# Kernel tuning notes

Measured on AMD Instinct MI355X. Metric: run time of the kernel, lower is better.

## Reference

```python
import jax, jax.numpy as jnp
import numpy as np

EPS = 1e-3  # tfa GroupNormalization default epsilon
H = 8       # num heads


def group_norm(x, gamma, beta):
    # x: [..., E]; per-sample group norm over each group of head_dim channels
    lead, E = x.shape[:-1], x.shape[-1]
    D = E // H
    xg = x.reshape(lead + (H, D))
    mu = xg.mean(-1, keepdims=True)
    var = xg.var(-1, keepdims=True)
    xg = (xg - mu) * jax.lax.rsqrt(var + EPS)
    xg = xg * gamma.reshape(H, D) + beta.reshape(H, D)
    return xg.reshape(lead + (E,))


def in_proj(x, W, b, gamma, beta):
    # Dense -> CELU(alpha=1) == ELU -> GroupNorm(groups=H)
    return group_norm(jax.nn.elu(x @ W + b), gamma, beta)


def setup_inputs() -> dict:
    B, M, E, MID = 16, 2048, 1024, 64
    D = E // H
    ks = jax.random.split(jax.random.key(0), 16)
    w = lambda k, shape: jax.random.normal(k, shape, jnp.float32) * 0.02
    inp = {
        "query": jax.random.normal(ks[0], (B, E), jnp.float32),
        "key": jax.random.normal(ks[1], (B * M, E), jnp.float32),
        "mask": jnp.ones((B, M), jnp.float32),
        "value1": jax.random.normal(ks[2], (B, E), jnp.float32),
        "value2": jax.random.normal(ks[3], (B * M, E), jnp.float32),
        # four in-projection layers: Dense(E,E) + GroupNorm gamma/beta
        "Wq": w(ks[4], (E, E)), "bq": jnp.zeros((E,), jnp.float32), "gq": jnp.ones((E,), jnp.float32), "Bq": jnp.zeros((E,), jnp.float32),
        "Wk": w(ks[5], (E, E)), "bk": jnp.zeros((E,), jnp.float32), "gk": jnp.ones((E,), jnp.float32), "Bk": jnp.zeros((E,), jnp.float32),
        "Wv1": w(ks[6], (E, E)), "bv1": jnp.zeros((E,), jnp.float32), "gv1": jnp.ones((E,), jnp.float32), "Bv1": jnp.zeros((E,), jnp.float32),
        "Wv2": w(ks[7], (E, E)), "bv2": jnp.zeros((E,), jnp.float32), "gv2": jnp.ones((E,), jnp.float32), "Bv2": jnp.zeros((E,), jnp.float32),
        # XLASCAtt: basic Dense(head_dim->64)+ReLU; last Dense(64->1); last2 Dense(64->head_dim)
        "Wb": w(ks[8], (D, MID)), "bb": jnp.zeros((MID,), jnp.float32),
        "Wl1": w(ks[9], (MID, 1)), "bl1": jnp.zeros((1,), jnp.float32),
        "Wl2": w(ks[10], (MID, D)), "bl2": jnp.zeros((D,), jnp.float32),
    }
    return inp


def reference(query, key, mask, value1, value2,
              Wq, bq, gq, Bq, Wk, bk, gk, Bk,
              Wv1, bv1, gv1, Bv1, Wv2, bv2, gv2, Bv2,
              Wb, bb, Wl1, bl1, Wl2, bl2):
    B, E = query.shape
    D = E // H
    # in-projections
    q = in_proj(query, Wq, bq, gq, Bq).reshape(B, H, D)            # [B,H,D]
    v1 = in_proj(value1, Wv1, bv1, gv1, Bv1).reshape(B, H, D)      # [B,H,D]
    k = in_proj(key, Wk, bk, gk, Bk).reshape(B, -1, H, D).transpose(0, 2, 1, 3)       # [B,H,M,D]
    v2 = in_proj(value2, Wv2, bv2, gv2, Bv2).reshape(B, -1, H, D).transpose(0, 2, 1, 3)  # [B,H,M,D]

    # low-rank bilinear attention map: elementwise q*k per head
    att_map = q[:, :, None, :] * k                                 # [B,H,M,D]
    basic = jax.nn.relu(att_map @ Wb + bb)                         # [B,H,M,MID]

    # masked mean-pool over memory positions
    m_ext = mask[:, None, :, None]                                 # [B,1,M,1]
    pool = (basic * m_ext).sum(-2) / m_ext.sum(-2)                 # [B,H,MID]

    # spatial attention (softmax over M) and channel gate (sigmoid)
    alpha_sp = (basic @ Wl1 + bl1)[..., 0]                         # [B,H,M]
    alpha_sp = jnp.where(mask[:, None, :] == 0, -1e9, alpha_sp)
    alpha_sp = jax.nn.softmax(alpha_sp, axis=-1)
    alpha_ch = jax.nn.sigmoid(pool @ Wl2 + bl2)                    # [B,H,D]

    v2_agg = jnp.einsum('bhm,bhmd->bhd', alpha_sp, v2)             # [B,H,D]
    attn = v1 * v2_agg * alpha_ch                                  # [B,H,D]
    return attn.reshape(B, H * D)
```

## Files before the change

kernel.cpp:

```cpp
#include <hip/hip_runtime.h>
#include <hip/hip_bf16.h>
#include <math.h>

typedef __attribute__((ext_vector_type(8))) short bf16x8;
typedef __attribute__((ext_vector_type(4))) float f32x4;
typedef __attribute__((ext_vector_type(8))) unsigned short u16x8;

typedef const float* fptr;
typedef const unsigned short* bfp;

__device__ inline float b2f(unsigned short u) {
    union { unsigned int i; float f; } v; v.i = ((unsigned int)u) << 16; return v.f;
}
__device__ inline unsigned short f2b(float x) {
    __hip_bfloat16 h = __float2bfloat16(x);
    return *(unsigned short*)&h;
}
__device__ inline float elu_f(float x) { return x > 0.f ? x : __expf(x) - 1.f; }

__device__ inline void load_lds16(const void* g, void* l) {
    __builtin_amdgcn_global_load_lds(
        (const __attribute__((address_space(1))) unsigned int*)g,
        (__attribute__((address_space(3))) unsigned int*)l, 16, 0, 0);
}

__global__ __launch_bounds__(256) void prep(
    fptr key, fptr value2, unsigned short* AbfK, unsigned short* AbfV2,
    fptr Wk, fptr Wv2, unsigned short* WtK, unsigned short* WtV2,
    fptr Wb, unsigned short* Wbt,
    fptr query, fptr Wq, fptr bq, fptr gq, fptr Bq,
    fptr value1, fptr Wv1, fptr bv1, fptr gv1, fptr Bv1,
    float* qws, float* v1ws)
{
    __shared__ __align__(16) char smem[16640];
    int blk = blockIdx.x, t = threadIdx.x;

    if (blk == 0) {
        unsigned short* tb = (unsigned short*)smem;
        for (int i = 0; i < 32; i++) {
            int idx = i * 256 + t;
            tb[(idx & 63) * 128 + (idx >> 6)] = f2b(Wb[idx]);
        }
        __syncthreads();
        for (int i = 0; i < 4; i++) {
            int o = (i * 256 + t) * 8;
            *(u16x8*)&Wbt[o] = *(const u16x8*)&tb[o];
        }
        return;
    }
    if (blk < 257) {
        float* xs = (float*)smem;
        float (*part)[128] = (float (*)[128])(smem + 4096);
        float (*r4)[2] = (float (*)[2])(smem + 4096 + 1024);
        int idx = blk - 1;
        int hgrp = idx & 7;
        int row  = (idx >> 3) & 15;
        int which = idx >> 7;
        fptr x  = which ? value1 : query;
        fptr W  = which ? Wv1 : Wq;
        fptr bi = which ? bv1 : bq;
        fptr g  = which ? gv1 : gq;
        fptr be = which ? Bv1 : Bq;
        float* outp = which ? v1ws : qws;
        int lane = t & 63, wv = t >> 6;
        for (int i = t; i < 1024; i += 256) xs[i] = x[row * 1024 + i];
        __syncthreads();
        int cl = t & 127, kh = t >> 7;
        int col = hgrp * 128 + cl;
        float acc = 0.f;
        const float* wp = W + (size_t)(kh * 512) * 1024 + col;
        for (int k = 0; k < 512; k++) acc += xs[kh * 512 + k] * wp[(size_t)k * 1024];
        part[kh][cl] = acc;
        __syncthreads();
        float e = 0.f;
        if (t < 128) e = elu_f(part[0][t] + part[1][t] + bi[col]);
        float s = e, ss = e * e;
        for (int m = 32; m > 0; m >>= 1) { s += __shfl_xor(s, m); ss += __shfl_xor(ss, m); }
        if (lane == 0) { r4[wv][0] = s; r4[wv][1] = ss; }
        __syncthreads();
        float S  = r4[0][0] + r4[1][0] + r4[2][0] + r4[3][0];
        float SS = r4[0][1] + r4[1][1] + r4[2][1] + r4[3][1];
        float mean = S * (1.f / 128.f);
        float var  = SS * (1.f / 128.f) - mean * mean;
        float inv  = rsqrtf(var + 1e-3f);
        if (t < 128) outp[row * 1024 + col] = (e - mean) * inv * g[col] + be[col];
        return;
    }
    if (blk < 769) {
        float (*tl)[65] = (float (*)[65])smem;
        int idx = blk - 257;
        fptr W = (idx >> 8) ? Wv2 : Wk;
        unsigned short* Wt = (idx >> 8) ? WtV2 : WtK;
        int k0 = ((idx >> 4) & 15) * 64, n0 = (idx & 15) * 64;
        #pragma unroll
        for (int i = 0; i < 16; i++) {
            int kl = i * 4 + (t >> 6), nl = t & 63;
            tl[kl][nl] = W[(size_t)(k0 + kl) * 1024 + n0 + nl];
        }
        __syncthreads();
        #pragma unroll
        for (int i = 0; i < 2; i++) {
            int nl = i * 32 + (t >> 3), kl8 = (t & 7) * 8;
            u16x8 o;
            #pragma unroll
            for (int e = 0; e < 8; e++) o[e] = f2b(tl[kl8 + e][nl]);
            *(u16x8*)&Wt[(size_t)(n0 + nl) * 1024 + k0 + kl8] = o;
        }
        return;
    }
    {
        int idx = blk - 769;
        fptr A = (idx < 2048) ? key : value2;
        unsigned short* Bp = (idx < 2048) ? AbfK : AbfV2;
        size_t base = (size_t)(idx & 2047) * 16384 + (size_t)t * 8;
        #pragma unroll
        for (int i = 0; i < 8; i++) {
            size_t e = base + (size_t)i * 2048;
            const float4* ap = (const float4*)(A + e);
            float4 a0 = ap[0], a1 = ap[1];
            u16x8 p = { f2b(a0.x), f2b(a0.y), f2b(a0.z), f2b(a0.w),
                        f2b(a1.x), f2b(a1.y), f2b(a1.z), f2b(a1.w) };
            *(u16x8*)(Bp + e) = p;
        }
    }
}

__global__ __launch_bounds__(256, 4) void gemm_fused(
    bfp AK, bfp WtK, fptr bkp, fptr gkp, fptr Bkp,
    bfp AV, bfp WtV, fptr bvp, fptr gvp, fptr Bvp,
    bfp Wbt, const float* qws, fptr maskp, fptr bbp, fptr Wl1, fptr bl1,
    float* logits, float* poolpart, __hip_bfloat16* Z)
{
    __shared__ __align__(16) unsigned short pool[17408];
    unsigned short (*As)[128][32] = (unsigned short (*)[128][32])pool;
    unsigned short (*Bs)[128][32] = (unsigned short (*)[128][32])(pool + 8192);
    unsigned short (*Tt)[136]     = (unsigned short (*)[136])pool;
    __shared__ float sstat[128][2][2];
    __shared__ float masksh[128];
    __shared__ float poolred[4][64];

    int bid = blockIdx.x;
    int xcd = bid & 7;
    int seq = bid >> 3;
    int grp = seq >> 3;
    int h   = seq & 7;
    int which = grp >> 5;
    int rowtile = xcd * 32 + (grp & 31);

    int r0 = rowtile * 128;
    int n0 = h * 128;
    int b  = r0 >> 11;
    int mloc = r0 & 2047;
    int mt = rowtile & 15;
    int t = threadIdx.x, lane = t & 63, w = t >> 6;
    int c = lane & 15, q = lane >> 4;
    int rowbase = (w & 1) * 64, colbase = (w >> 1) * 64;

    bfp A    = which ? AV  : AK;
    bfp Wt   = which ? WtV : WtK;
    fptr bias = which ? bvp : bkp;
    fptr g    = which ? gvp : gkp;
    fptr be   = which ? Bvp : Bkp;

    if (which == 0 && t < 128) masksh[t] = maskp[r0 + t];

    f32x4 acc[4][4];
    const f32x4 fzero = {0.f, 0.f, 0.f, 0.f};
    #pragma unroll
    for (int i = 0; i < 4; i++)
        #pragma unroll
        for (int j = 0; j < 4; j++) acc[i][j] = fzero;

    int srow = lane >> 2;
    int sseg = (lane & 3) * 8;
    const unsigned short* ag = A  + (size_t)(r0 + w * 32 + srow) * 1024 + sseg;
    const unsigned short* bg = Wt + (size_t)(n0 + w * 32 + srow) * 1024 + sseg;

    for (int k0 = 0; k0 < 1024; k0 += 64) {
        load_lds16(ag + k0,                  &As[0][w * 32][0]);
        load_lds16(ag + k0 + 16 * 1024,      &As[0][w * 32 + 16][0]);
        load_lds16(ag + k0 + 32,             &As[1][w * 32][0]);
        load_lds16(ag + k0 + 32 + 16 * 1024, &As[1][w * 32 + 16][0]);
        load_lds16(bg + k0,                  &Bs[0][w * 32][0]);
        load_lds16(bg + k0 + 16 * 1024,      &Bs[0][w * 32 + 16][0]);
        load_lds16(bg + k0 + 32,             &Bs[1][w * 32][0]);
        load_lds16(bg + k0 + 32 + 16 * 1024, &Bs[1][w * 32 + 16][0]);
        __syncthreads();
        #pragma unroll
        for (int p = 0; p < 2; p++) {
            bf16x8 af[4], bfv[4];
            #pragma unroll
            for (int i = 0; i < 4; i++) af[i]  = *(const bf16x8*)&As[p][rowbase + i * 16 + c][q * 8];
            #pragma unroll
            for (int j = 0; j < 4; j++) bfv[j] = *(const bf16x8*)&Bs[p][colbase + j * 16 + c][q * 8];
            #pragma unroll
            for (int i = 0; i < 4; i++)
                #pragma unroll
                for (int j = 0; j < 4; j++)
                    acc[i][j] = __builtin_amdgcn_mfma_f32_16x16x32_bf16(af[i], bfv[j], acc[i][j], 0, 0, 0);
        }
        __syncthreads();
    }

    float bcol[4], gcol[4], Bcol[4];
    #pragma unroll
    for (int j = 0; j < 4; j++) {
        int cg = n0 + colbase + j * 16 + c;
        bcol[j] = bias[cg]; gcol[j] = g[cg]; Bcol[j] = be[cg];
    }
    #pragma unroll
    for (int i = 0; i < 4; i++)
        #pragma unroll
        for (int j = 0; j < 4; j++)
            #pragma unroll
            for (int r = 0; r < 4; r++)
                acc[i][j][r] = elu_f(acc[i][j][r] + bcol[j]);
    #pragma unroll
    for (int i = 0; i < 4; i++) {
        #pragma unroll
        for (int r = 0; r < 4; r++) {
            float s  = acc[i][0][r] + acc[i][1][r] + acc[i][2][r] + acc[i][3][r];
            float ss = acc[i][0][r] * acc[i][0][r] + acc[i][1][r] * acc[i][1][r]
                     + acc[i][2][r] * acc[i][2][r] + acc[i][3][r] * acc[i][3][r];
            for (int m = 1; m < 16; m <<= 1) { s += __shfl_xor(s, m); ss += __shfl_xor(ss, m); }
            if (c == 0) {
                int rl = rowbase + i * 16 + q * 4 + r;
                sstat[rl][w >> 1][0] = s;
                sstat[rl][w >> 1][1] = ss;
            }
        }
    }
    __syncthreads();
    #pragma unroll
    for (int i = 0; i < 4; i++) {
        #pragma unroll
        for (int r = 0; r < 4; r++) {
            int rl = rowbase + i * 16 + q * 4 + r;
            float S  = sstat[rl][0][0] + sstat[rl][1][0];
            float SS = sstat[rl][0][1] + sstat[rl][1][1];
            float mean = S * (1.f / 128.f);
            float var  = SS * (1.f / 128.f) - mean * mean;
            float inv  = rsqrtf(var + 1e-3f);
            #pragma unroll
            for (int j = 0; j < 4; j++) {
                int cl = colbase + j * 16 + c;
                float v = (acc[i][j][r] - mean) * inv * gcol[j] + Bcol[j];
                Tt[rl][cl] = f2b(v);
            }
        }
    }
    __syncthreads();
    if (which != 0) {
        unsigned short* Zu = (unsigned short*)Z;
        #pragma unroll
        for (int i = 0; i < 8; i++) {
            int idx2 = i * 256 + t;
            int row = idx2 >> 4, ch = (idx2 & 15) * 8;
            *(u16x8*)&Zu[(size_t)(r0 + row) * 1024 + n0 + ch] = *(const u16x8*)&Tt[row][ch];
        }
        return;
    }

    const float* qrow = qws + b * 1024 + h * 128;
    f32x4 acc2[2][4];
    #pragma unroll
    for (int i = 0; i < 2; i++)
        #pragma unroll
        for (int j = 0; j < 4; j++) acc2[i][j] = fzero;
    #pragma unroll
    for (int s = 0; s < 4; s++) {
        bf16x8 af2[2], bfv[4];
        float qv[8];
        #pragma unroll
        for (int e = 0; e < 8; e++) qv[e] = qrow[s * 32 + q * 8 + e];
        #pragma unroll
        for (int i = 0; i < 2; i++)
            af2[i] = *(const bf16x8*)&Tt[w * 32 + i * 16 + c][s * 32 + q * 8];
        #pragma unroll
        for (int j = 0; j < 4; j++) {
            bf16x8 wv = *(const bf16x8*)&Wbt[(j * 16 + c) * 128 + s * 32 + q * 8];
            bf16x8 bv;
            #pragma unroll
            for (int e = 0; e < 8; e++)
                bv[e] = (short)f2b(b2f((unsigned short)wv[e]) * qv[e]);
            bfv[j] = bv;
        }
        #pragma unroll
        for (int i = 0; i < 2; i++)
            #pragma unroll
            for (int j = 0; j < 4; j++)
                acc2[i][j] = __builtin_amdgcn_mfma_f32_16x16x32_bf16(af2[i], bfv[j], acc2[i][j], 0, 0, 0);
    }

    float bbs[4], wl1s[4];
    #pragma unroll
    for (int j = 0; j < 4; j++) { bbs[j] = bbp[j * 16 + c]; wl1s[j] = Wl1[j * 16 + c]; }
    float bl1v = bl1[0];
    float pp[4] = {0.f, 0.f, 0.f, 0.f};
    #pragma unroll
    for (int i = 0; i < 2; i++) {
        #pragma unroll
        for (int r = 0; r < 4; r++) {
            int ml = w * 32 + i * 16 + q * 4 + r;
            float mv = masksh[ml];
            float lg = 0.f;
            #pragma unroll
            for (int j = 0; j < 4; j++) {
                float basic = fmaxf(acc2[i][j][r] + bbs[j], 0.f);
                lg += basic * wl1s[j];
                pp[j] += basic * mv;
            }
            lg += __shfl_xor(lg, 1); lg += __shfl_xor(lg, 2);
            lg += __shfl_xor(lg, 4); lg += __shfl_xor(lg, 8);
            if (c == 0)
                logits[((size_t)(b * 8 + h)) * 2048 + mloc + ml] = lg + bl1v;
        }
    }
    #pragma unroll
    for (int j = 0; j < 4; j++) {
        pp[j] += __shfl_xor(pp[j], 16);
        pp[j] += __shfl_xor(pp[j], 32);
    }
    if (lane < 16) {
        #pragma unroll
        for (int j = 0; j < 4; j++) poolred[w][j * 16 + c] = pp[j];
    }
    __syncthreads();
    if (t < 64) {
        float p = poolred[0][t] + poolred[1][t] + poolred[2][t] + poolred[3][t];
        poolpart[((size_t)((b * 8 + h) * 16 + mt)) * 64 + t] = p;
    }
}

__global__ __launch_bounds__(512) void finalize_fused(
    const float* logits, const float* poolpart, fptr maskp,
    const __hip_bfloat16* v2buf, const float* v1ws,
    fptr Wl2, fptr bl2, float* out)
{
    __shared__ float alph[2048];
    __shared__ float red[8];
    __shared__ float redm[8];
    __shared__ float pools[64];
    __shared__ float ach[128];
    __shared__ float redl[8][128];
    int h = blockIdx.x, b = blockIdx.y;
    int t = threadIdx.x, lane = t & 63, wv = t >> 6;

    const float* lg = logits + (size_t)(b * 8 + h) * 2048;
    float msum_l = 0.f, mx_l = -1e30f;
    for (int i = t; i < 2048; i += 512) {
        float mv = maskp[b * 2048 + i];
        msum_l += mv;
        float v = (mv == 0.f) ? -1e9f : lg[i];
        alph[i] = v;
        mx_l = fmaxf(mx_l, v);
    }
    for (int mm = 32; mm > 0; mm >>= 1) {
        msum_l += __shfl_xor(msum_l, mm);
        mx_l = fmaxf(mx_l, __shfl_xor(mx_l, mm));
    }
    if (lane == 0) { red[wv] = msum_l; redm[wv] = mx_l; }
    __syncthreads();
    float msum = 0.f, mx = -1e30f;
    #pragma unroll
    for (int i = 0; i < 8; i++) { msum += red[i]; mx = fmaxf(mx, redm[i]); }

    float se = 0.f;
    for (int i = t; i < 2048; i += 512) {
        float e = __expf(alph[i] - mx);
        alph[i] = e;
        se += e;
    }
    for (int mm = 32; mm > 0; mm >>= 1) se += __shfl_xor(se, mm);
    __syncthreads();
    if (lane == 0) red[wv] = se;
    __syncthreads();
    float S = 0.f;
    #pragma unroll
    for (int i = 0; i < 8; i++) S += red[i];
    float invS = 1.f / S;
    for (int i = t; i < 2048; i += 512) alph[i] *= invS;

    if (t < 64) {
        const float* pq = poolpart + ((size_t)(b * 8 + h) * 16) * 64 + t;
        float p = 0.f;
        for (int pt = 0; pt < 16; pt++) p += pq[pt * 64];
        pools[t] = p / msum;
    }
    __syncthreads();
    if (t < 128) {
        float s2 = bl2[t];
        for (int mid = 0; mid < 64; mid++) s2 += pools[mid] * Wl2[mid * 128 + t];
        ach[t] = 1.f / (1.f + __expf(-s2));
    }
    __syncthreads();

    int mo = lane >> 4, d8 = (lane & 15) * 8;
    float acc[8] = {};
    for (int it = 0; it < 64; it++) {
        int m = it * 32 + wv * 4 + mo;
        bf16x8 v8 = *(const bf16x8*)&v2buf[((size_t)(b * 2048 + m)) * 1024 + h * 128 + d8];
        float a = alph[m];
        #pragma unroll
        for (int j = 0; j < 8; j++)
            acc[j] += a * b2f(((unsigned short*)&v8)[j]);
    }
    #pragma unroll
    for (int j = 0; j < 8; j++) {
        acc[j] += __shfl_xor(acc[j], 16);
        acc[j] += __shfl_xor(acc[j], 32);
    }
    if (lane < 16) {
        #pragma unroll
        for (int j = 0; j < 8; j++) redl[wv][d8 + j] = acc[j];
    }
    __syncthreads();
    if (t < 128) {
        float s = 0.f;
        #pragma unroll
        for (int i = 0; i < 8; i++) s += redl[i][t];
        out[b * 1024 + h * 128 + t] = v1ws[b * 1024 + h * 128 + t] * s * ach[t];
    }
}

extern "C" void kernel_launch(void* const* d_in, const int* in_sizes, int n_in,
                              void* d_out, int out_size, void* d_ws, size_t ws_size,
                              hipStream_t stream) {
    fptr query  = (fptr)d_in[0];
    fptr key    = (fptr)d_in[1];
    fptr maskp  = (fptr)d_in[2];
    fptr value1 = (fptr)d_in[3];
    fptr value2 = (fptr)d_in[4];
    fptr Wq = (fptr)d_in[5],  bq = (fptr)d_in[6],  gq = (fptr)d_in[7],  Bq = (fptr)d_in[8];
    fptr Wk = (fptr)d_in[9],  bk = (fptr)d_in[10], gk = (fptr)d_in[11], Bk = (fptr)d_in[12];
    fptr Wv1 = (fptr)d_in[13], bv1 = (fptr)d_in[14], gv1 = (fptr)d_in[15], Bv1 = (fptr)d_in[16];
    fptr Wv2 = (fptr)d_in[17], bv2 = (fptr)d_in[18], gv2 = (fptr)d_in[19], Bv2 = (fptr)d_in[20];
    fptr Wb = (fptr)d_in[21], bb = (fptr)d_in[22];
    fptr Wl1 = (fptr)d_in[23], bl1 = (fptr)d_in[24];
    fptr Wl2 = (fptr)d_in[25], bl2 = (fptr)d_in[26];

    const size_t MB = 1024 * 1024;
    char* w = (char*)d_ws;
    unsigned short* AbfK  = (unsigned short*)w;
    unsigned short* AbfV2 = (unsigned short*)(w + 64 * MB);
    __hip_bfloat16* zV2   = (__hip_bfloat16*)(w + 128 * MB);
    unsigned short* WtK   = (unsigned short*)(w + 192 * MB);
    unsigned short* WtV2  = (unsigned short*)(w + 194 * MB);
    unsigned short* Wbt   = (unsigned short*)(w + 196 * MB);
    float* qws      = (float*)(w + 196 * MB + 65536 + 2 * MB);
    float* v1ws     = qws + 16 * 1024;
    float* logits   = v1ws + 16 * 1024;
    float* poolpart = logits + 16 * 8 * 2048;
    float* out = (float*)d_out;

    hipLaunchKernelGGL(prep, dim3(4865), dim3(256), 0, stream,
                       key, value2, AbfK, AbfV2,
                       Wk, Wv2, WtK, WtV2, Wb, Wbt,
                       query, Wq, bq, gq, Bq, value1, Wv1, bv1, gv1, Bv1,
                       qws, v1ws);
    hipLaunchKernelGGL(gemm_fused, dim3(4096), dim3(256), 0, stream,
                       (bfp)AbfK, (bfp)WtK, bk, gk, Bk,
                       (bfp)AbfV2, (bfp)WtV2, bv2, gv2, Bv2,
                       (bfp)Wbt, qws, maskp, bb, Wl1, bl1, logits, poolpart, zV2);
    hipLaunchKernelGGL(finalize_fused, dim3(8, 16), dim3(512), 0, stream,
                       logits, poolpart, maskp, zV2, v1ws, Wl2, bl2, out);
}
```

Before: 565.7 us.

## Fuse fp32-to-bf16 activation conversion into GEMM A-tile loads

Removes the separate prep pass that converted key and value2 from fp32 to bf16 into workspace buffers. The GEMM now reads fp32 A tiles directly, converts them in registers and stores them to LDS, while B still uses direct global-to-LDS loads. This cuts a full extra read/write pass over both large activations and shrinks the prep grid. In exchange, each GEMM block loads twice as many A bytes, and A goes through registers instead of async LDS loads. Because A is reused across the 8 head tiles, the extra traffic may be served from cache.

```diff
diff --git a/kernel.cpp b/kernel.cpp
--- a/kernel.cpp
+++ b/kernel.cpp
@@ -25,7 +25,6 @@
 }
 
 __global__ __launch_bounds__(256) void prep(
-    fptr key, fptr value2, unsigned short* AbfK, unsigned short* AbfV2,
     fptr Wk, fptr Wv2, unsigned short* WtK, unsigned short* WtV2,
     fptr Wb, unsigned short* Wbt,
     fptr query, fptr Wq, fptr bq, fptr gq, fptr Bq,
@@ -86,7 +85,7 @@
         if (t < 128) outp[row * 1024 + col] = (e - mean) * inv * g[col] + be[col];
         return;
     }
-    if (blk < 769) {
+    {
         float (*tl)[65] = (float (*)[65])smem;
         int idx = blk - 257;
         fptr W = (idx >> 8) ? Wv2 : Wk;
@@ -106,28 +105,12 @@
             for (int e = 0; e < 8; e++) o[e] = f2b(tl[kl8 + e][nl]);
             *(u16x8*)&Wt[(size_t)(n0 + nl) * 1024 + k0 + kl8] = o;
         }
-        return;
-    }
-    {
-        int idx = blk - 769;
-        fptr A = (idx < 2048) ? key : value2;
-        unsigned short* Bp = (idx < 2048) ? AbfK : AbfV2;
-        size_t base = (size_t)(idx & 2047) * 16384 + (size_t)t * 8;
-        #pragma unroll
-        for (int i = 0; i < 8; i++) {
-            size_t e = base + (size_t)i * 2048;
-            const float4* ap = (const float4*)(A + e);
-            float4 a0 = ap[0], a1 = ap[1];
-            u16x8 p = { f2b(a0.x), f2b(a0.y), f2b(a0.z), f2b(a0.w),
-                        f2b(a1.x), f2b(a1.y), f2b(a1.z), f2b(a1.w) };
-            *(u16x8*)(Bp + e) = p;
-        }
     }
 }
 
 __global__ __launch_bounds__(256, 4) void gemm_fused(
-    bfp AK, bfp WtK, fptr bkp, fptr gkp, fptr Bkp,
-    bfp AV, bfp WtV, fptr bvp, fptr gvp, fptr Bvp,
+    fptr AKf, bfp WtK, fptr bkp, fptr gkp, fptr Bkp,
+    fptr AVf, bfp WtV, fptr bvp, fptr gvp, fptr Bvp,
     bfp Wbt, const float* qws, fptr maskp, fptr bbp, fptr Wl1, fptr bl1,
     float* logits, float* poolpart, __hip_bfloat16* Z)
 {
@@ -156,8 +139,8 @@
     int c = lane & 15, q = lane >> 4;
     int rowbase = (w & 1) * 64, colbase = (w >> 1) * 64;
 
-    bfp A    = which ? AV  : AK;
-    bfp Wt   = which ? WtV : WtK;
+    fptr Af   = which ? AVf : AKf;
+    bfp Wt    = which ? WtV : WtK;
     fptr bias = which ? bvp : bkp;
     fptr g    = which ? gvp : gkp;
     fptr be   = which ? Bvp : Bkp;
@@ -173,18 +156,23 @@
 
     int srow = lane >> 2;
     int sseg = (lane & 3) * 8;
-    const unsigned short* ag = A  + (size_t)(r0 + w * 32 + srow) * 1024 + sseg;
+    const float* agf = Af + (size_t)(r0 + w * 32 + srow) * 1024 + sseg;
     const unsigned short* bg = Wt + (size_t)(n0 + w * 32 + srow) * 1024 + sseg;
 
     for (int k0 = 0; k0 < 1024; k0 += 64) {
-        load_lds16(ag + k0,                  &As[0][w * 32][0]);
-        load_lds16(ag + k0 + 16 * 1024,      &As[0][w * 32 + 16][0]);
-        load_lds16(ag + k0 + 32,             &As[1][w * 32][0]);
-        load_lds16(ag + k0 + 32 + 16 * 1024, &As[1][w * 32 + 16][0]);
         load_lds16(bg + k0,                  &Bs[0][w * 32][0]);
         load_lds16(bg + k0 + 16 * 1024,      &Bs[0][w * 32 + 16][0]);
         load_lds16(bg + k0 + 32,             &Bs[1][w * 32][0]);
         load_lds16(bg + k0 + 32 + 16 * 1024, &Bs[1][w * 32 + 16][0]);
+        #pragma unroll
+        for (int ch = 0; ch < 4; ch++) {
+            const float* src = agf + k0 + (ch & 1) * 16 * 1024 + (ch >> 1) * 32;
+            float4 f0 = *(const float4*)src;
+            float4 f1 = *(const float4*)(src + 4);
+            u16x8 hv = { f2b(f0.x), f2b(f0.y), f2b(f0.z), f2b(f0.w),
+                         f2b(f1.x), f2b(f1.y), f2b(f1.z), f2b(f1.w) };
+            *(u16x8*)&As[ch >> 1][w * 32 + (ch & 1) * 16 + srow][sseg] = hv;
+        }
         __syncthreads();
         #pragma unroll
         for (int p = 0; p < 2; p++) {
@@ -441,26 +429,23 @@
 
     const size_t MB = 1024 * 1024;
     char* w = (char*)d_ws;
-    unsigned short* AbfK  = (unsigned short*)w;
-    unsigned short* AbfV2 = (unsigned short*)(w + 64 * MB);
-    __hip_bfloat16* zV2   = (__hip_bfloat16*)(w + 128 * MB);
-    unsigned short* WtK   = (unsigned short*)(w + 192 * MB);
-    unsigned short* WtV2  = (unsigned short*)(w + 194 * MB);
-    unsigned short* Wbt   = (unsigned short*)(w + 196 * MB);
-    float* qws      = (float*)(w + 196 * MB + 65536 + 2 * MB);
+    __hip_bfloat16* zV2   = (__hip_bfloat16*)w;
+    unsigned short* WtK   = (unsigned short*)(w + 64 * MB);
+    unsigned short* WtV2  = (unsigned short*)(w + 66 * MB);
+    unsigned short* Wbt   = (unsigned short*)(w + 68 * MB);
+    float* qws      = (float*)(w + 68 * MB + 65536);
     float* v1ws     = qws + 16 * 1024;
     float* logits   = v1ws + 16 * 1024;
     float* poolpart = logits + 16 * 8 * 2048;
     float* out = (float*)d_out;
 
-    hipLaunchKernelGGL(prep, dim3(4865), dim3(256), 0, stream,
-                       key, value2, AbfK, AbfV2,
+    hipLaunchKernelGGL(prep, dim3(769), dim3(256), 0, stream,
                        Wk, Wv2, WtK, WtV2, Wb, Wbt,
                        query, Wq, bq, gq, Bq, value1, Wv1, bv1, gv1, Bv1,
                        qws, v1ws);
     hipLaunchKernelGGL(gemm_fused, dim3(4096), dim3(256), 0, stream,
-                       (bfp)AbfK, (bfp)WtK, bk, gk, Bk,
-                       (bfp)AbfV2, (bfp)WtV2, bv2, gv2, Bv2,
+                       key, (bfp)WtK, bk, gk, Bk,
+                       value2, (bfp)WtV2, bv2, gv2, Bv2,
                        (bfp)Wbt, qws, maskp, bb, Wl1, bl1, logits, poolpart, zV2);
     hipLaunchKernelGGL(finalize_fused, dim3(8, 16), dim3(512), 0, stream,
                        logits, poolpart, maskp, zV2, v1ws, Wl2, bl2, out);
```

Result: faster. 529.9 us (-6.3%).
